# Optimization experiments

Measured on AMD Instinct MI355X. Metric: run time of the kernel, lower is better.

The kernel has to match this reference:

```python
import jax, jax.numpy as jnp
import numpy as np

N_GROUPS = 4


def setup_inputs() -> dict:
    key = jax.random.key(0)
    k1, k2 = jax.random.split(key)
    x = jax.random.normal(k1, (64, 256, 32, 32), dtype=jnp.float32)
    # codebook: (group_size, num_embeddings) = (256 // 4, 512), torch.rand init
    weight = jax.random.uniform(k2, (64, 512), dtype=jnp.float32)
    return {"x": x, "weight": weight}


def _group_quantize(xg, emb):
    # xg: (B, g, H, W), emb: (g, K)
    # squared Euclidean distance; argmin is identical to argmin of torch.norm
    d2 = (jnp.sum(xg * xg, axis=1)[..., None]
          - 2.0 * jnp.einsum('bghw,gk->bhwk', xg, emb)
          + jnp.sum(emb * emb, axis=0))        # (B, H, W, K)
    argmin = jnp.argmin(d2, axis=-1)            # (B, H, W)
    result = jnp.transpose(emb.T[argmin], (0, 3, 1, 2))  # (B, g, H, W)
    return result, argmin


def reference(x, weight):
    B, D, H, W = x.shape
    g = D // N_GROUPS
    results = []
    argmins = []
    for i in range(N_GROUPS):  # fixed small structural loop
        r, a = _group_quantize(x[:, i * g:(i + 1) * g], weight)
        results.append(r)
        argmins.append(a)
    result = jnp.concatenate(results, axis=1) / jnp.sqrt(jnp.float32(N_GROUPS))
    argmins = jnp.stack(argmins, axis=1)  # (B, n_groups, H, W)
    return result, argmins
```

## Files before the change

### kernel.cpp

```cpp
#include <hip/hip_runtime.h>
#include <float.h>

#define KCODES 512
#define GDIM 64
#define TAU 4.0e-3f

typedef __attribute__((ext_vector_type(8))) short short8;
typedef __attribute__((ext_vector_type(4))) float floatx4;


__device__ __forceinline__ void bf16split(float x, short& hi, short& lo) {
    unsigned u = __float_as_uint(x);
    unsigned h = (u + 0x7fffu + ((u >> 16) & 1u)) >> 16;
    hi = (short)h;
    float hf = __uint_as_float(h << 16);
    float l = x - hf;
    unsigned ul = __float_as_uint(l);
    lo = (short)((ul + 0x7fffu + ((ul >> 16) & 1u)) >> 16);
}

__device__ __forceinline__ void gload_lds16(const void* g, void* l) {
    __builtin_amdgcn_global_load_lds(
        (const __attribute__((address_space(1))) void*)g,
        (__attribute__((address_space(3))) void*)l, 16, 0, 0);
}

__launch_bounds__(256)
__global__ void prep_kernel(const float* __restrict__ w,
                            float* __restrict__ embT,
                            float* __restrict__ e2,
                            double* __restrict__ e2d,
                            short* __restrict__ emb_hi,
                            short* __restrict__ emb_lo) {
    int t = blockIdx.x * 256 + threadIdx.x;
    int k = t >> 6;
    int g = t & 63;
    float v = w[(size_t)g * KCODES + k];
    embT[(size_t)k * GDIM + g] = v;
    short h, l; bf16split(-2.0f * v, h, l);
    emb_hi[(size_t)k * GDIM + g] = h;
    emb_lo[(size_t)k * GDIM + g] = l;
    float s = v * v;
    double sd = (double)v * (double)v;
#pragma unroll
    for (int off = 32; off > 0; off >>= 1) {
        s  += __shfl_xor(s, off, 64);
        sd += __shfl_xor(sd, off, 64);
    }
    if (g == 0) { e2[k] = s; e2d[k] = sd; }
}

__launch_bounds__(256, 1)
__global__ void vq_kernel(const float* __restrict__ x,
                          const float* __restrict__ embT,
                          const float* __restrict__ e2,
                          const double* __restrict__ e2d,
                          const short* __restrict__ emb_hi,
                          const short* __restrict__ emb_lo,
                          float* __restrict__ out_res,
                          float* __restrict__ out_arg) {
    __shared__ short s_hi[2][64 * 64];
    __shared__ short s_lo[2][64 * 64];
    __shared__ float s_e2[512];
    __shared__ int   s_arg[128];
    __shared__ float s_fixx[4][64];
    __shared__ int   s_flags[128];
    __shared__ int   s_nflag;

    const int t = threadIdx.x;
    const int wid = t >> 6;
    const int lane = t & 63;
    const int q = lane >> 4;
    const int c = lane & 15;
    const int blk = blockIdx.x;
    const int grp = blk >> 9;
    const int posbase = ((blk & 511) << 7) + wid * 32;
    const int b = posbase >> 10;
    const int hwb = posbase & 1023;

    if (t == 0) s_nflag = 0;

    const int rA = wid * 16 + (lane >> 3);
    const int rB = rA + 8;
    const int uA = (lane & 7) ^ (lane >> 3);
    const int srcA = rA * 64 + uA * 8;
    const int srcB = rB * 64 + uA * 8;

#define PREFETCH(CH, BUF)                                                      \
    {                                                                          \
        const short* gh_ = emb_hi + (size_t)(CH) * 4096;                       \
        const short* gl_ = emb_lo + (size_t)(CH) * 4096;                       \
        gload_lds16(gh_ + srcA, &s_hi[BUF][wid * 1024]);                       \
        gload_lds16(gh_ + srcB, &s_hi[BUF][wid * 1024 + 512]);                 \
        gload_lds16(gl_ + srcA, &s_lo[BUF][wid * 1024]);                       \
        gload_lds16(gl_ + srcB, &s_lo[BUF][wid * 1024 + 512]);                 \
    }

    PREFETCH(0, 0);
    s_e2[t] = e2[t];
    s_e2[t + 256] = e2[t + 256];

    const float* xbase = x + (size_t)b * 262144 + (size_t)grp * 65536 + hwb;

    short8 ahi[2][2], alo[2][2];
#pragma unroll
    for (int mt = 0; mt < 2; ++mt)
#pragma unroll
        for (int kt = 0; kt < 2; ++kt) {
#pragma unroll
            for (int j = 0; j < 8; ++j) {
                float xv = xbase[(kt * 32 + q * 8 + j) * 1024 + mt * 16 + c];
                short h, l; bf16split(xv, h, l);
                ahi[mt][kt][j] = h; alo[mt][kt][j] = l;
            }
        }

    float best[2][4], sec[2][4]; int arg[2][4];
#pragma unroll
    for (int mt = 0; mt < 2; ++mt)
#pragma unroll
        for (int r = 0; r < 4; ++r) { best[mt][r] = FLT_MAX; sec[mt][r] = FLT_MAX; arg[mt][r] = 0; }

    const int p8 = (q ^ (c & 7)) << 3;

    __syncthreads();

    int cur = 0;
    for (int ch = 0; ch < 8; ++ch) {
        if (ch < 7) PREFETCH(ch + 1, cur ^ 1);
        const int C0 = ch * 64;

#pragma unroll
        for (int nt = 0; nt < 4; ++nt) {
            const int o = (nt * 16 + c) * 64 + p8;
            short8 bh0 = *(const short8*)&s_hi[cur][o];
            short8 bh1 = *(const short8*)&s_hi[cur][o ^ 32];
            short8 bl0 = *(const short8*)&s_lo[cur][o];
            short8 bl1 = *(const short8*)&s_lo[cur][o ^ 32];
            const float se2 = s_e2[C0 + nt * 16 + c];
            const int   n   = C0 + nt * 16 + c;
#pragma unroll
            for (int mt = 0; mt < 2; ++mt) {
                floatx4 a4 = (floatx4){se2, se2, se2, se2};
                a4 = __builtin_amdgcn_mfma_f32_16x16x32_bf16(alo[mt][0], bh0, a4, 0, 0, 0);
                a4 = __builtin_amdgcn_mfma_f32_16x16x32_bf16(ahi[mt][0], bl0, a4, 0, 0, 0);
                a4 = __builtin_amdgcn_mfma_f32_16x16x32_bf16(ahi[mt][0], bh0, a4, 0, 0, 0);
                a4 = __builtin_amdgcn_mfma_f32_16x16x32_bf16(alo[mt][1], bh1, a4, 0, 0, 0);
                a4 = __builtin_amdgcn_mfma_f32_16x16x32_bf16(ahi[mt][1], bl1, a4, 0, 0, 0);
                a4 = __builtin_amdgcn_mfma_f32_16x16x32_bf16(ahi[mt][1], bh1, a4, 0, 0, 0);
#pragma unroll
                for (int r = 0; r < 4; ++r) {
                    float s = a4[r];
                    float bo = best[mt][r];
                    best[mt][r] = fminf(bo, s);
                    arg[mt][r]  = (s < bo) ? n : arg[mt][r];
                    sec[mt][r]  = __builtin_amdgcn_fmed3f(bo, sec[mt][r], s);
                }
            }
        }

        __syncthreads();
        cur ^= 1;
    }

#pragma unroll
    for (int mt = 0; mt < 2; ++mt)
#pragma unroll
        for (int r = 0; r < 4; ++r) {
            float b_ = best[mt][r], s_ = sec[mt][r]; int n_ = arg[mt][r];
#pragma unroll
            for (int sh = 1; sh < 16; sh <<= 1) {
                float ob = __shfl_xor(b_, sh, 64);
                float os = __shfl_xor(s_, sh, 64);
                int   on = __shfl_xor(n_, sh, 64);
                float bo = b_;
                b_ = fminf(bo, ob);
                n_ = (ob < bo) ? on : n_;
                s_ = fminf(fminf(s_, os), fmaxf(bo, ob));
            }
            if (c == 0) {
                int p = mt * 16 + q * 4 + r;
                s_arg[wid * 32 + p] = n_;
                if (s_ - b_ <= TAU) {
                    int slot = atomicAdd(&s_nflag, 1);
                    s_flags[slot] = wid * 32 + p;
                }
            }
        }

    {
        int p = lane & 31, gi = lane >> 5;
        int ac = s_arg[wid * 32 + p];
        const float* ev = embT + (size_t)ac * GDIM;
        float* rp = out_res + (size_t)b * 262144 + (size_t)grp * 65536 + hwb + p;
#pragma unroll
        for (int it = 0; it < 32; ++it) {
            int g = it * 2 + gi;
            rp[(size_t)g * 1024] = ev[g] * 0.5f;
        }
    }

    __syncthreads();
    if (t < 128) {
        int bp = ((blk & 511) << 7) + t;
        out_arg[(size_t)(bp >> 10) * 4096 + (size_t)grp * 1024 + (bp & 1023)] =
            (float)s_arg[t];
    }
    __syncthreads();

    const int nf = s_nflag;
    for (int f = wid; f < nf; f += 4) {
        const int hwa = s_flags[f];
        const int pos = ((blk & 511) << 7) + hwa;
        const int fb = pos >> 10;
        const int sidx = pos & 1023;
        s_fixx[wid][lane] =
            x[(size_t)fb * 262144 + (size_t)grp * 65536 + (size_t)lane * 1024 + sidx];
        asm volatile("s_waitcnt lgkmcnt(0)" ::: "memory");

        double bd = DBL_MAX; int bk = 0;
        for (int m = 0; m < KCODES / 64; ++m) {
            const int k = lane + m * 64;
            const float* er = embT + (size_t)k * GDIM;
            double dot = 0.0;
#pragma unroll
            for (int g = 0; g < GDIM; g += 4) {
                float4 e4 = *(const float4*)(er + g);
                float4 xv = *(const float4*)&s_fixx[wid][g];
                dot += (double)xv.x * (double)e4.x;
                dot += (double)xv.y * (double)e4.y;
                dot += (double)xv.z * (double)e4.z;
                dot += (double)xv.w * (double)e4.w;
            }
            double s = e2d[k] - 2.0 * dot;
            if (s < bd) { bd = s; bk = k; }
        }
        for (int off = 32; off > 0; off >>= 1) {
            double od = __shfl_down(bd, off, 64);
            int    ok = __shfl_down(bk, off, 64);
            if (od < bd || (od == bd && ok < bk)) { bd = od; bk = ok; }
        }
        bk = __shfl(bk, 0, 64);

        if (lane == 0)
            out_arg[(size_t)fb * 4096 + (size_t)grp * 1024 + sidx] = (float)bk;
        out_res[(size_t)fb * 262144 + (size_t)grp * 65536 + (size_t)lane * 1024 + sidx] =
            embT[(size_t)bk * GDIM + lane] * 0.5f;
    }
#undef PREFETCH
}

extern "C" void kernel_launch(void* const* d_in, const int* in_sizes, int n_in,
                              void* d_out, int out_size, void* d_ws, size_t ws_size,
                              hipStream_t stream) {
    const float* x = (const float*)d_in[0];
    const float* w = (const float*)d_in[1];
    float* out_res = (float*)d_out;
    float* out_arg = (float*)d_out + 16777216;

    float*    embT   = (float*)d_ws;
    float*    e2     = embT + 32768;
    double*   e2d    = (double*)((char*)d_ws + (size_t)33280 * 4);
    short*    emb_hi = (short*)((float*)d_ws + 34304);
    short*    emb_lo = (short*)((float*)d_ws + 50688);

    prep_kernel<<<128, 256, 0, stream>>>(w, embT, e2, e2d, emb_hi, emb_lo);
    vq_kernel<<<2048, 256, 0, stream>>>(x, embT, e2, e2d, emb_hi, emb_lo,
                                        out_res, out_arg);
}
```

Before: 219.0 us.

## Pack distance and index into sortable uint keys; halve LDS chunks for occupancy

Adds a positive bias to the code norms so distances stay positive. Each distance is then packed with its code index in the low 9 mantissa bits into one unsigned key, so the argmin and second-best tracking become integer min/max without a separate index register. The LDS codebook chunk is halved to 32 codes over 16 iterations, and launch bounds are raised to 5 blocks per CU, aiming for more occupancy and lower register and LDS use. Truncating the mantissa loses precision, so the near-tie tolerance is widened, which sends more positions down the slow fp64 recheck path.

```diff
diff --git a/kernel.cpp b/kernel.cpp
--- a/kernel.cpp
+++ b/kernel.cpp
@@ -3,7 +3,8 @@
 
 #define KCODES 512
 #define GDIM 64
-#define TAU 4.0e-3f
+#define SBIAS 96.0f
+#define TAUQ 0.015f
 
 typedef __attribute__((ext_vector_type(8))) short short8;
 typedef __attribute__((ext_vector_type(4))) float floatx4;
@@ -50,7 +51,7 @@
     if (g == 0) { e2[k] = s; e2d[k] = sd; }
 }
 
-__launch_bounds__(256, 1)
+__launch_bounds__(256, 5)
 __global__ void vq_kernel(const float* __restrict__ x,
                           const float* __restrict__ embT,
                           const float* __restrict__ e2,
@@ -59,8 +60,8 @@
                           const short* __restrict__ emb_lo,
                           float* __restrict__ out_res,
                           float* __restrict__ out_arg) {
-    __shared__ short s_hi[2][64 * 64];
-    __shared__ short s_lo[2][64 * 64];
+    __shared__ short s_hi[2][32 * 64];
+    __shared__ short s_lo[2][32 * 64];
     __shared__ float s_e2[512];
     __shared__ int   s_arg[128];
     __shared__ float s_fixx[4][64];
@@ -80,25 +81,19 @@
 
     if (t == 0) s_nflag = 0;
 
-    const int rA = wid * 16 + (lane >> 3);
-    const int rB = rA + 8;
+    const int rA = wid * 8 + (lane >> 3);
     const int uA = (lane & 7) ^ (lane >> 3);
     const int srcA = rA * 64 + uA * 8;
-    const int srcB = rB * 64 + uA * 8;
 
 #define PREFETCH(CH, BUF)                                                      \
     {                                                                          \
-        const short* gh_ = emb_hi + (size_t)(CH) * 4096;                       \
-        const short* gl_ = emb_lo + (size_t)(CH) * 4096;                       \
-        gload_lds16(gh_ + srcA, &s_hi[BUF][wid * 1024]);                       \
-        gload_lds16(gh_ + srcB, &s_hi[BUF][wid * 1024 + 512]);                 \
-        gload_lds16(gl_ + srcA, &s_lo[BUF][wid * 1024]);                       \
-        gload_lds16(gl_ + srcB, &s_lo[BUF][wid * 1024 + 512]);                 \
+        gload_lds16(emb_hi + (size_t)(CH) * 2048 + srcA, &s_hi[BUF][wid * 512]); \
+        gload_lds16(emb_lo + (size_t)(CH) * 2048 + srcA, &s_lo[BUF][wid * 512]); \
     }
 
     PREFETCH(0, 0);
-    s_e2[t] = e2[t];
-    s_e2[t + 256] = e2[t + 256];
+    s_e2[t] = e2[t] + SBIAS;
+    s_e2[t + 256] = e2[t + 256] + SBIAS;
 
     const float* xbase = x + (size_t)b * 262144 + (size_t)grp * 65536 + hwb;
 
@@ -115,30 +110,30 @@
             }
         }
 
-    float best[2][4], sec[2][4]; int arg[2][4];
+    unsigned best[2][4], sec[2][4];
 #pragma unroll
     for (int mt = 0; mt < 2; ++mt)
 #pragma unroll
-        for (int r = 0; r < 4; ++r) { best[mt][r] = FLT_MAX; sec[mt][r] = FLT_MAX; arg[mt][r] = 0; }
+        for (int r = 0; r < 4; ++r) { best[mt][r] = 0xFFFFFFFFu; sec[mt][r] = 0xFFFFFFFFu; }
 
     const int p8 = (q ^ (c & 7)) << 3;
 
     __syncthreads();
 
     int cur = 0;
-    for (int ch = 0; ch < 8; ++ch) {
-        if (ch < 7) PREFETCH(ch + 1, cur ^ 1);
-        const int C0 = ch * 64;
-
-#pragma unroll
-        for (int nt = 0; nt < 4; ++nt) {
+    for (int ch = 0; ch < 16; ++ch) {
+        if (ch < 15) PREFETCH(ch + 1, cur ^ 1);
+        const int C0 = ch * 32;
+
+#pragma unroll
+        for (int nt = 0; nt < 2; ++nt) {
             const int o = (nt * 16 + c) * 64 + p8;
             short8 bh0 = *(const short8*)&s_hi[cur][o];
             short8 bh1 = *(const short8*)&s_hi[cur][o ^ 32];
             short8 bl0 = *(const short8*)&s_lo[cur][o];
             short8 bl1 = *(const short8*)&s_lo[cur][o ^ 32];
             const float se2 = s_e2[C0 + nt * 16 + c];
-            const int   n   = C0 + nt * 16 + c;
+            const unsigned n = (unsigned)(C0 + nt * 16 + c);
 #pragma unroll
             for (int mt = 0; mt < 2; ++mt) {
                 floatx4 a4 = (floatx4){se2, se2, se2, se2};
@@ -150,11 +145,11 @@
                 a4 = __builtin_amdgcn_mfma_f32_16x16x32_bf16(ahi[mt][1], bh1, a4, 0, 0, 0);
 #pragma unroll
                 for (int r = 0; r < 4; ++r) {
-                    float s = a4[r];
-                    float bo = best[mt][r];
-                    best[mt][r] = fminf(bo, s);
-                    arg[mt][r]  = (s < bo) ? n : arg[mt][r];
-                    sec[mt][r]  = __builtin_amdgcn_fmed3f(bo, sec[mt][r], s);
+                    unsigned key = (__float_as_uint(a4[r]) & ~511u) | n;
+                    unsigned bo = best[mt][r];
+                    best[mt][r] = bo < key ? bo : key;
+                    unsigned mx = bo > key ? bo : key;
+                    sec[mt][r]  = sec[mt][r] < mx ? sec[mt][r] : mx;
                 }
             }
         }
@@ -167,21 +162,22 @@
     for (int mt = 0; mt < 2; ++mt)
 #pragma unroll
         for (int r = 0; r < 4; ++r) {
-            float b_ = best[mt][r], s_ = sec[mt][r]; int n_ = arg[mt][r];
+            unsigned b_ = best[mt][r], s_ = sec[mt][r];
 #pragma unroll
             for (int sh = 1; sh < 16; sh <<= 1) {
-                float ob = __shfl_xor(b_, sh, 64);
-                float os = __shfl_xor(s_, sh, 64);
-                int   on = __shfl_xor(n_, sh, 64);
-                float bo = b_;
-                b_ = fminf(bo, ob);
-                n_ = (ob < bo) ? on : n_;
-                s_ = fminf(fminf(s_, os), fmaxf(bo, ob));
+                unsigned ob = (unsigned)__shfl_xor((int)b_, sh, 64);
+                unsigned os = (unsigned)__shfl_xor((int)s_, sh, 64);
+                unsigned mx = b_ > ob ? b_ : ob;
+                s_ = s_ < os ? s_ : os;
+                s_ = s_ < mx ? s_ : mx;
+                b_ = b_ < ob ? b_ : ob;
             }
             if (c == 0) {
                 int p = mt * 16 + q * 4 + r;
-                s_arg[wid * 32 + p] = n_;
-                if (s_ - b_ <= TAU) {
+                s_arg[wid * 32 + p] = (int)(b_ & 511u);
+                float fb = __uint_as_float(b_ & ~511u);
+                float fs = __uint_as_float(s_ & ~511u);
+                if (fs - fb <= TAUQ) {
                     int slot = atomicAdd(&s_nflag, 1);
                     s_flags[slot] = wid * 32 + p;
                 }
@@ -223,7 +219,7 @@
             const int k = lane + m * 64;
             const float* er = embT + (size_t)k * GDIM;
             double dot = 0.0;
-#pragma unroll
+#pragma unroll 4
             for (int g = 0; g < GDIM; g += 4) {
                 float4 e4 = *(const float4*)(er + g);
                 float4 xv = *(const float4*)&s_fixx[wid][g];
```

After: 247.8 us. 13.2% more time.

## Fuse codebook preprocessing into the VQ kernel and drop the prep launch

Applied to the files above, without the earlier changes.

Removes the separate prep kernel. Each block now loads raw codebook columns from the weight tensor, splits them into bf16 hi/lo, computes squared norms with LDS atomics, and writes the staged tiles into LDS inside the double-buffered chunk loop. This saves one kernel launch and the workspace round-trip. In exchange, every one of the 2048 blocks redoes the conversion and norm math and issues strided global loads in place of direct global-to-LDS copies. The float32 norm summation order also changes, and the exact-fix path now reads the untransposed weights with strided access.

```diff
diff --git a/kernel.cpp b/kernel.cpp
--- a/kernel.cpp
+++ b/kernel.cpp
@@ -7,7 +7,6 @@
 
 typedef __attribute__((ext_vector_type(8))) short short8;
 typedef __attribute__((ext_vector_type(4))) float floatx4;
-
 
 __device__ __forceinline__ void bf16split(float x, short& hi, short& lo) {
     unsigned u = __float_as_uint(x);
@@ -19,44 +18,9 @@
     lo = (short)((ul + 0x7fffu + ((ul >> 16) & 1u)) >> 16);
 }
 
-__device__ __forceinline__ void gload_lds16(const void* g, void* l) {
-    __builtin_amdgcn_global_load_lds(
-        (const __attribute__((address_space(1))) void*)g,
-        (__attribute__((address_space(3))) void*)l, 16, 0, 0);
-}
-
-__launch_bounds__(256)
-__global__ void prep_kernel(const float* __restrict__ w,
-                            float* __restrict__ embT,
-                            float* __restrict__ e2,
-                            double* __restrict__ e2d,
-                            short* __restrict__ emb_hi,
-                            short* __restrict__ emb_lo) {
-    int t = blockIdx.x * 256 + threadIdx.x;
-    int k = t >> 6;
-    int g = t & 63;
-    float v = w[(size_t)g * KCODES + k];
-    embT[(size_t)k * GDIM + g] = v;
-    short h, l; bf16split(-2.0f * v, h, l);
-    emb_hi[(size_t)k * GDIM + g] = h;
-    emb_lo[(size_t)k * GDIM + g] = l;
-    float s = v * v;
-    double sd = (double)v * (double)v;
-#pragma unroll
-    for (int off = 32; off > 0; off >>= 1) {
-        s  += __shfl_xor(s, off, 64);
-        sd += __shfl_xor(sd, off, 64);
-    }
-    if (g == 0) { e2[k] = s; e2d[k] = sd; }
-}
-
 __launch_bounds__(256, 1)
 __global__ void vq_kernel(const float* __restrict__ x,
-                          const float* __restrict__ embT,
-                          const float* __restrict__ e2,
-                          const double* __restrict__ e2d,
-                          const short* __restrict__ emb_hi,
-                          const short* __restrict__ emb_lo,
+                          const float* __restrict__ w,
                           float* __restrict__ out_res,
                           float* __restrict__ out_arg) {
     __shared__ short s_hi[2][64 * 64];
@@ -79,26 +43,43 @@
     const int hwb = posbase & 1023;
 
     if (t == 0) s_nflag = 0;
-
-    const int rA = wid * 16 + (lane >> 3);
-    const int rB = rA + 8;
-    const int uA = (lane & 7) ^ (lane >> 3);
-    const int srcA = rA * 64 + uA * 8;
-    const int srcB = rB * 64 + uA * 8;
-
-#define PREFETCH(CH, BUF)                                                      \
+    s_e2[t] = 0.0f;
+    s_e2[t + 256] = 0.0f;
+
+    const int j  = t & 63;
+    const int qq = t >> 6;
+    const int u0 = (((2 * qq)     ^ (j & 7)) << 3);
+    const int u1 = (((2 * qq + 1) ^ (j & 7)) << 3);
+    const float* wbase = w + (size_t)(qq * 16) * KCODES + j;
+
+#define STAGE_WRITE(BUF, C0)                                                   \
     {                                                                          \
-        const short* gh_ = emb_hi + (size_t)(CH) * 4096;                       \
-        const short* gl_ = emb_lo + (size_t)(CH) * 4096;                       \
-        gload_lds16(gh_ + srcA, &s_hi[BUF][wid * 1024]);                       \
-        gload_lds16(gh_ + srcB, &s_hi[BUF][wid * 1024 + 512]);                 \
-        gload_lds16(gl_ + srcA, &s_lo[BUF][wid * 1024]);                       \
-        gload_lds16(gl_ + srcB, &s_lo[BUF][wid * 1024 + 512]);                 \
-    }
-
-    PREFETCH(0, 0);
-    s_e2[t] = e2[t];
-    s_e2[t + 256] = e2[t + 256];
+        short8 hA, hB, lA, lB;                                                 \
+        float e2p = 0.0f;                                                      \
+        _Pragma("unroll")                                                      \
+        for (int i = 0; i < 8; ++i) {                                          \
+            short h_, l_;                                                      \
+            bf16split(-2.0f * wv[i], h_, l_);                                  \
+            hA[i] = h_; lA[i] = l_;                                            \
+            e2p = __fmaf_rn(wv[i], wv[i], e2p);                                \
+        }                                                                      \
+        _Pragma("unroll")                                                      \
+        for (int i = 0; i < 8; ++i) {                                          \
+            short h_, l_;                                                      \
+            bf16split(-2.0f * wv[8 + i], h_, l_);                              \
+            hB[i] = h_; lB[i] = l_;                                            \
+            e2p = __fmaf_rn(wv[8 + i], wv[8 + i], e2p);                        \
+        }                                                                      \
+        *(short8*)&s_hi[BUF][j * 64 + u0] = hA;                                \
+        *(short8*)&s_hi[BUF][j * 64 + u1] = hB;                                \
+        *(short8*)&s_lo[BUF][j * 64 + u0] = lA;                                \
+        *(short8*)&s_lo[BUF][j * 64 + u1] = lB;                                \
+        atomicAdd(&s_e2[(C0) + j], e2p);                                       \
+    }
+
+    float wv[16];
+#pragma unroll
+    for (int i = 0; i < 16; ++i) wv[i] = wbase[i * KCODES];
 
     const float* xbase = x + (size_t)b * 262144 + (size_t)grp * 65536 + hwb;
 
@@ -108,10 +89,10 @@
 #pragma unroll
         for (int kt = 0; kt < 2; ++kt) {
 #pragma unroll
-            for (int j = 0; j < 8; ++j) {
-                float xv = xbase[(kt * 32 + q * 8 + j) * 1024 + mt * 16 + c];
+            for (int jj = 0; jj < 8; ++jj) {
+                float xv = xbase[(kt * 32 + q * 8 + jj) * 1024 + mt * 16 + c];
                 short h, l; bf16split(xv, h, l);
-                ahi[mt][kt][j] = h; alo[mt][kt][j] = l;
+                ahi[mt][kt][jj] = h; alo[mt][kt][jj] = l;
             }
         }
 
@@ -123,11 +104,16 @@
 
     const int p8 = (q ^ (c & 7)) << 3;
 
+    __syncthreads();
+    STAGE_WRITE(0, 0);
     __syncthreads();
 
     int cur = 0;
     for (int ch = 0; ch < 8; ++ch) {
-        if (ch < 7) PREFETCH(ch + 1, cur ^ 1);
+        if (ch < 7) {
+#pragma unroll
+            for (int i = 0; i < 16; ++i) wv[i] = wbase[i * KCODES + (ch + 1) * 64];
+        }
         const int C0 = ch * 64;
 
 #pragma unroll
@@ -159,6 +145,8 @@
             }
         }
 
+        if (ch < 7) STAGE_WRITE(cur ^ 1, C0 + 64);
+
         __syncthreads();
         cur ^= 1;
     }
@@ -191,12 +179,11 @@
     {
         int p = lane & 31, gi = lane >> 5;
         int ac = s_arg[wid * 32 + p];
-        const float* ev = embT + (size_t)ac * GDIM;
         float* rp = out_res + (size_t)b * 262144 + (size_t)grp * 65536 + hwb + p;
 #pragma unroll
         for (int it = 0; it < 32; ++it) {
             int g = it * 2 + gi;
-            rp[(size_t)g * 1024] = ev[g] * 0.5f;
+            rp[(size_t)g * 1024] = w[(size_t)g * KCODES + ac] * 0.5f;
         }
     }
 
@@ -221,18 +208,19 @@
         double bd = DBL_MAX; int bk = 0;
         for (int m = 0; m < KCODES / 64; ++m) {
             const int k = lane + m * 64;
-            const float* er = embT + (size_t)k * GDIM;
-            double dot = 0.0;
+            double d0 = 0.0, d1 = 0.0, d2 = 0.0, d3 = 0.0;
 #pragma unroll
             for (int g = 0; g < GDIM; g += 4) {
-                float4 e4 = *(const float4*)(er + g);
-                float4 xv = *(const float4*)&s_fixx[wid][g];
-                dot += (double)xv.x * (double)e4.x;
-                dot += (double)xv.y * (double)e4.y;
-                dot += (double)xv.z * (double)e4.z;
-                dot += (double)xv.w * (double)e4.w;
-            }
-            double s = e2d[k] - 2.0 * dot;
+                double e0 = (double)w[(size_t)(g + 0) * KCODES + k];
+                double e1 = (double)w[(size_t)(g + 1) * KCODES + k];
+                double e2v = (double)w[(size_t)(g + 2) * KCODES + k];
+                double e3 = (double)w[(size_t)(g + 3) * KCODES + k];
+                d0 += e0 * (e0 - 2.0 * (double)s_fixx[wid][g + 0]);
+                d1 += e1 * (e1 - 2.0 * (double)s_fixx[wid][g + 1]);
+                d2 += e2v * (e2v - 2.0 * (double)s_fixx[wid][g + 2]);
+                d3 += e3 * (e3 - 2.0 * (double)s_fixx[wid][g + 3]);
+            }
+            double s = (d0 + d1) + (d2 + d3);
             if (s < bd) { bd = s; bk = k; }
         }
         for (int off = 32; off > 0; off >>= 1) {
@@ -245,9 +233,9 @@
         if (lane == 0)
             out_arg[(size_t)fb * 4096 + (size_t)grp * 1024 + sidx] = (float)bk;
         out_res[(size_t)fb * 262144 + (size_t)grp * 65536 + (size_t)lane * 1024 + sidx] =
-            embT[(size_t)bk * GDIM + lane] * 0.5f;
-    }
-#undef PREFETCH
+            w[(size_t)lane * KCODES + bk] * 0.5f;
+    }
+#undef STAGE_WRITE
 }
 
 extern "C" void kernel_launch(void* const* d_in, const int* in_sizes, int n_in,
@@ -257,14 +245,7 @@
     const float* w = (const float*)d_in[1];
     float* out_res = (float*)d_out;
     float* out_arg = (float*)d_out + 16777216;
-
-    float*    embT   = (float*)d_ws;
-    float*    e2     = embT + 32768;
-    double*   e2d    = (double*)((char*)d_ws + (size_t)33280 * 4);
-    short*    emb_hi = (short*)((float*)d_ws + 34304);
-    short*    emb_lo = (short*)((float*)d_ws + 50688);
-
-    prep_kernel<<<128, 256, 0, stream>>>(w, embT, e2, e2d, emb_hi, emb_lo);
-    vq_kernel<<<2048, 256, 0, stream>>>(x, embT, e2, e2d, emb_hi, emb_lo,
-                                        out_res, out_arg);
+    (void)d_ws; (void)ws_size;
+
+    vq_kernel<<<2048, 256, 0, stream>>>(x, w, out_res, out_arg);
 }
```

Result: slower. 228.1 us (+4.2%).
